# Performance work log

Measured on AMD Instinct MI355X. Metric: run time of the kernel, lower is better.

The kernel has to match this reference:

```python
import jax, jax.numpy as jnp
import numpy as np

NH, DH, DM = 16, 128, 2048
ROPE_THETA = 10000.0


def setup_inputs() -> dict:
    key = jax.random.key(0)
    k1, k2, k3 = jax.random.split(key, 3)
    x = jax.random.normal(k1, (2, 2048, DM), dtype=jnp.float32)
    w_qkv = jax.random.normal(k2, (3 * DM, DM), dtype=jnp.float32) * (DM ** -0.5)
    w_op = jax.random.normal(k3, (DM, DM), dtype=jnp.float32) * (DM ** -0.5)
    return {"x": x, "w_qkv": w_qkv, "w_op": w_op}


def _rope_tables(T, dtype):
    inv_freq = 1.0 / (ROPE_THETA ** (jnp.arange(0, DH, 2, dtype=jnp.float32) / DH))
    t = jnp.arange(T, dtype=jnp.float32)
    freqs = jnp.outer(t, inv_freq)              # (T, DH/2)
    emb = jnp.concatenate([freqs, freqs], axis=-1)  # (T, DH)
    cos = jnp.cos(emb)[None, :, None, :].astype(dtype)  # (1,T,1,DH)
    sin = jnp.sin(emb)[None, :, None, :].astype(dtype)
    return cos, sin


def _rotate_half(a):
    a1, a2 = a[..., : DH // 2], a[..., DH // 2 :]
    return jnp.concatenate([-a2, a1], axis=-1)


def reference(x, w_qkv, w_op):
    B, T, D = x.shape
    qkv = jnp.einsum('btd,ed->bte', x, w_qkv).reshape(B, T, 3, NH, DH)
    q, k, v = qkv[:, :, 0], qkv[:, :, 1], qkv[:, :, 2]  # (B,T,NH,DH)

    cos, sin = _rope_tables(T, x.dtype)
    q = q * cos + _rotate_half(q) * sin
    k = k * cos + _rotate_half(k) * sin

    # causal scaled dot-product attention
    scale = 1.0 / jnp.sqrt(jnp.asarray(DH, dtype=x.dtype))
    scores = jnp.einsum('bqhd,bkhd->bhqk', q, k) * scale  # (B,NH,T,T)
    causal = jnp.tril(jnp.ones((T, T), dtype=bool))
    scores = jnp.where(causal[None, None], scores, jnp.asarray(-1e30, dtype=x.dtype))
    attn = jax.nn.softmax(scores, axis=-1)
    out = jnp.einsum('bhqk,bkhd->bqhd', attn, v).reshape(B, T, D)
    return jnp.einsum('btd,ed->bte', out, w_op)
```

## Files before the change

### kernel.cpp

```cpp
#include <hip/hip_runtime.h>
#include <hip/hip_bf16.h>
#include <cstdint>

#define NHEAD 16
#define DHEAD 128
#define DMODEL 2048
#define TSEQ 2048
#define BATCH 2

using bf16 = __hip_bfloat16;
typedef __attribute__((ext_vector_type(4))) float  f32x4;
typedef __attribute__((ext_vector_type(2))) float  f32x2;
typedef __attribute__((ext_vector_type(4))) float  float4_t;
typedef __attribute__((ext_vector_type(4))) short  s16x4;
typedef __bf16 bf16x8 __attribute__((ext_vector_type(8)));

#define GLOAD_LDS16(gptr, lptr)                                                        \
  __builtin_amdgcn_global_load_lds((const __attribute__((address_space(1))) void*)(gptr), \
                                   (__attribute__((address_space(3))) void*)(lptr), 16, 0, 0)

#if __has_builtin(__builtin_amdgcn_exp2f)
#define EXP2(x) __builtin_amdgcn_exp2f(x)
#else
#define EXP2(x) exp2f(x)
#endif

__device__ __forceinline__ float bf2f(bf16 v) { return __bfloat162float(v); }
__device__ __forceinline__ bf16  f2bf(float f) { return __float2bfloat16(f); }
__device__ __forceinline__ unsigned short bfbits(float f) {
  return __builtin_bit_cast(unsigned short, f2bf(f));
}
__device__ __forceinline__ unsigned int pack2(float a, float b) {
  return (unsigned int)bfbits(a) | ((unsigned int)bfbits(b) << 16);
}

__global__ void cast_f32_to_bf16(const float* __restrict__ in, unsigned short* __restrict__ out, int n4) {
  int stride = gridDim.x * blockDim.x;
  for (int i = blockIdx.x * blockDim.x + threadIdx.x; i < n4; i += stride) {
    float4_t v = reinterpret_cast<const float4_t*>(in)[i];
    s16x4 r;
    r.x = (short)bfbits(v.x);
    r.y = (short)bfbits(v.y);
    r.z = (short)bfbits(v.z);
    r.w = (short)bfbits(v.w);
    reinterpret_cast<s16x4*>(out)[i] = r;
  }
}

__global__ void rope_tables(f32x2* __restrict__ cstab) {
  int i = blockIdx.x * blockDim.x + threadIdx.x;
  if (i >= TSEQ * 64) return;
  int t = i >> 6, f = i & 63;
  float inv = __expf(-((2.0f * (float)f) / 128.0f) * logf(10000.0f));
  float ang = (float)t * inv;
  f32x2 cs;
  cs.x = cosf(ang);
  cs.y = sinf(ang);
  cstab[i] = cs;
}

__global__ void transpose_v(const unsigned short* __restrict__ qkv, unsigned short* __restrict__ vt) {
  __shared__ short tile[64][132];
  const int bh = blockIdx.y;
  const int b = bh >> 4, h = bh & 15;
  const int t0 = blockIdx.x * 64;
  const int tid = threadIdx.x;
#pragma unroll
  for (int p = 0; p < 8; ++p) {
    int row  = p * 8 + (tid >> 5);
    int col  = (tid & 31) * 4;
    const unsigned short* src = qkv + (size_t)(b * TSEQ + t0 + row) * (3 * DMODEL) + 2 * DMODEL + h * DHEAD + col;
    s16x4 v = *reinterpret_cast<const s16x4*>(src);
    *reinterpret_cast<s16x4*>(&tile[row][col]) = v;
  }
  __syncthreads();
#pragma unroll
  for (int q = 0; q < 8; ++q) {
    int idx = q * 256 + tid;
    int d = idx >> 4, tq = idx & 15;
    s16x4 r;
    r.x = tile[tq * 4 + 0][d];
    r.y = tile[tq * 4 + 1][d];
    r.z = tile[tq * 4 + 2][d];
    r.w = tile[tq * 4 + 3][d];
    *reinterpret_cast<s16x4*>(vt + (size_t)(bh * DHEAD + d) * TSEQ + t0 + tq * 4) = r;
  }
}

__device__ __forceinline__ void store_c(float* p, float v) { *p = v; }
__device__ __forceinline__ void store_c(unsigned short* p, float v) { *p = bfbits(v); }

template <typename CT, bool ROPE>
__global__ __launch_bounds__(256, 2) void gemm_bt(const unsigned short* __restrict__ A,
                                                  const unsigned short* __restrict__ B,
                                                  CT* __restrict__ C, int M, int N, int K,
                                                  const f32x2* __restrict__ cstab) {
  __shared__ unsigned short As[128 * 32];
  __shared__ unsigned short Bs[128 * 32];
  const int tid  = threadIdx.x;
  const int wave = tid >> 6, lane = tid & 63;
  const int m0 = blockIdx.x * 128, n0 = blockIdx.y * 128;
  const int wm = wave * 32;
  const int lrow = lane >> 4, lcol = lane & 15;
  f32x4 acc[2][8] = {};

  for (int k0 = 0; k0 < K; k0 += 32) {
#pragma unroll
    for (int it = 0; it < 2; ++it) {
      int chunk = wave * 2 + it;
      int eoff  = chunk * 512 + lane * 8;
      int row   = eoff >> 5, col = eoff & 31;
      GLOAD_LDS16(A + (size_t)(m0 + row) * K + k0 + col, As + chunk * 512);
      GLOAD_LDS16(B + (size_t)(n0 + row) * K + k0 + col, Bs + chunk * 512);
    }
    __syncthreads();
    bf16x8 af[2], bfr[8];
#pragma unroll
    for (int mi = 0; mi < 2; ++mi)
      af[mi] = *reinterpret_cast<const bf16x8*>(&As[(wm + mi * 16 + lcol) * 32 + lrow * 8]);
#pragma unroll
    for (int ni = 0; ni < 8; ++ni)
      bfr[ni] = *reinterpret_cast<const bf16x8*>(&Bs[(ni * 16 + lcol) * 32 + lrow * 8]);
#pragma unroll
    for (int mi = 0; mi < 2; ++mi)
#pragma unroll
      for (int ni = 0; ni < 8; ++ni)
        acc[mi][ni] = __builtin_amdgcn_mfma_f32_16x16x32_bf16(af[mi], bfr[ni], acc[mi][ni], 0, 0, 0);
    __syncthreads();
  }

  if (ROPE && n0 < 2 * DMODEL) {
    const float qsc = (n0 < DMODEL) ? 0.12751743f : 1.0f;
#pragma unroll
    for (int mi = 0; mi < 2; ++mi)
#pragma unroll
      for (int j = 0; j < 4; ++j) {
        const int r = m0 + wm + mi * 16 + lrow * 4 + j;
        const int t = r & (TSEQ - 1);
#pragma unroll
        for (int ni = 0; ni < 4; ++ni) {
          const int f = ni * 16 + lcol;
          const f32x2 cs = cstab[t * 64 + f];
          const float a1 = acc[mi][ni][j];
          const float a2 = acc[mi][ni + 4][j];
          store_c(C + (size_t)r * N + n0 + f,      (a1 * cs.x - a2 * cs.y) * qsc);
          store_c(C + (size_t)r * N + n0 + f + 64, (a2 * cs.x + a1 * cs.y) * qsc);
        }
      }
  } else {
#pragma unroll
    for (int mi = 0; mi < 2; ++mi)
#pragma unroll
      for (int ni = 0; ni < 8; ++ni)
#pragma unroll
        for (int j = 0; j < 4; ++j) {
          int r = m0 + wm + mi * 16 + lrow * 4 + j;
          int c = n0 + ni * 16 + lcol;
          store_c(C + (size_t)r * N + c, acc[mi][ni][j]);
        }
  }
}

__global__ __launch_bounds__(512, 4) void flash_attn(const unsigned short* __restrict__ qkv,
                                                     const unsigned short* __restrict__ vt,
                                                     unsigned short* __restrict__ out) {
  __shared__ unsigned short kb[2][64 * 128];
  __shared__ unsigned short vb[2][128 * 64];
  __shared__ unsigned short plds[8][16 * 64];

  const int tid  = threadIdx.x;
  const int wave = tid >> 6, lane = tid & 63;
  const int lrow = lane >> 4, lcol = lane & 15;
  const int h = blockIdx.y, b = blockIdx.z;
  const int q0b = blockIdx.x * 128;
  const int q0w = q0b + wave * 16;
  const size_t qkbase = (size_t)b * TSEQ * (3 * DMODEL);
  const unsigned short* kptr = qkv + qkbase + DMODEL + h * DHEAD;
  const unsigned short* vptr = vt + (size_t)((b * NHEAD + h) * DHEAD) * TSEQ;

  bf16x8 qf[4];
#pragma unroll
  for (int kk = 0; kk < 4; ++kk)
    qf[kk] = *reinterpret_cast<const bf16x8*>(
        qkv + qkbase + (size_t)(q0w + lcol) * (3 * DMODEL) + h * DHEAD + kk * 32 + lrow * 8);

  f32x4 o[8] = {};
  float m = -1.0e30f, l = 0.f;

  const int nsteps = 2 * blockIdx.x + 2;

#define STAGE_KV(bi, kv0s)                                                              \
  {                                                                                     \
    _Pragma("unroll")                                                                   \
    for (int c = 0; c < 2; ++c) {                                                       \
      int cc = c * 512 + tid;                                                           \
      int krow = cc >> 4, kchk = (cc & 15) ^ (krow & 7);                                \
      GLOAD_LDS16(kptr + (size_t)((kv0s) + krow) * (3 * DMODEL) + kchk * 8,             \
                  &kb[bi][cc * 8]);                                                     \
      int vrow = cc >> 3, vchk = (cc & 7) ^ (vrow & 7);                                 \
      GLOAD_LDS16(vptr + (size_t)vrow * TSEQ + (kv0s) + vchk * 8,                       \
                  &vb[bi][cc * 8]);                                                     \
    }                                                                                   \
  }

  STAGE_KV(0, 0);
  __syncthreads();

  int cur = 0;
  for (int s = 0; s < nsteps; ++s) {
    const int kv0 = s * 64;
    if (s + 1 < nsteps) STAGE_KV(cur ^ 1, kv0 + 64);

    if (kv0 <= q0w + 15) {
      const unsigned short* kbc = kb[cur];
      const unsigned short* vbc = vb[cur];

      f32x4 sc[4] = {};
      __builtin_amdgcn_s_setprio(1);
#pragma unroll
      for (int n = 0; n < 4; ++n) {
        const int r = n * 16 + lcol;
#pragma unroll
        for (int kk = 0; kk < 4; ++kk) {
          bf16x8 kf = *reinterpret_cast<const bf16x8*>(
              &kbc[r * 128 + (((kk * 4 + lrow) ^ (lcol & 7)) << 3)]);
          sc[n] = __builtin_amdgcn_mfma_f32_16x16x32_bf16(kf, qf[kk], sc[n], 0, 0, 0);
        }
      }
      __builtin_amdgcn_s_setprio(0);

      const bool diag = (kv0 + 63 > q0w);
      const int qi = q0w + lcol;
      float sv[16];
#pragma unroll
      for (int n = 0; n < 4; ++n)
#pragma unroll
        for (int j = 0; j < 4; ++j) {
          float v = sc[n][j];
          if (diag && (kv0 + n * 16 + lrow * 4 + j) > qi) v = -1.0e30f;
          sv[n * 4 + j] = v;
        }
      float t8[8];
#pragma unroll
      for (int j = 0; j < 8; ++j) t8[j] = fmaxf(sv[j], sv[j + 8]);
#pragma unroll
      for (int j = 0; j < 4; ++j) t8[j] = fmaxf(t8[j], t8[j + 4]);
      float pm = fmaxf(fmaxf(t8[0], t8[1]), fmaxf(t8[2], t8[3]));
      pm = fmaxf(pm, __shfl_xor(pm, 16));
      pm = fmaxf(pm, __shfl_xor(pm, 32));

      if (__any(pm > m + 11.5f)) {
        const float mn  = fmaxf(m, pm);
        const float fsc = EXP2(m - mn);
        m = mn;
        l *= fsc;
#pragma unroll
        for (int c = 0; c < 8; ++c) o[c] *= fsc;
      }

#pragma unroll
      for (int i = 0; i < 16; ++i) sv[i] = EXP2(sv[i] - m);
      float a8[8];
#pragma unroll
      for (int j = 0; j < 8; ++j) a8[j] = sv[j] + sv[j + 8];
#pragma unroll
      for (int j = 0; j < 4; ++j) a8[j] += a8[j + 4];
      float rs = (a8[0] + a8[1]) + (a8[2] + a8[3]);
      rs += __shfl_xor(rs, 16);
      rs += __shfl_xor(rs, 32);
      l += rs;

      char* pw = reinterpret_cast<char*>(&plds[wave][0]);
#pragma unroll
      for (int n = 0; n < 4; ++n)
#pragma unroll
        for (int j = 0; j < 4; j += 2) {
          int boff = (lcol << 7) + ((((n << 1) + (lrow >> 1)) ^ (lcol & 7)) << 4) +
                     ((lrow & 1) << 3) + (j << 1);
          *reinterpret_cast<unsigned int*>(pw + boff) = pack2(sv[n * 4 + j], sv[n * 4 + j + 1]);
        }
      asm volatile("s_waitcnt lgkmcnt(0)" ::: "memory");

      bf16x8 pf0 = *reinterpret_cast<const bf16x8*>(
          pw + (lcol << 7) + ((lrow ^ (lcol & 7)) << 4));
      bf16x8 pf1 = *reinterpret_cast<const bf16x8*>(
          pw + (lcol << 7) + (((4 + lrow) ^ (lcol & 7)) << 4));

      __builtin_amdgcn_s_setprio(1);
#pragma unroll
      for (int c = 0; c < 8; ++c) {
        const int d = c * 16 + lcol;
        bf16x8 vf0 = *reinterpret_cast<const bf16x8*>(
            &vbc[d * 64 + ((lrow ^ (lcol & 7)) << 3)]);
        o[c] = __builtin_amdgcn_mfma_f32_16x16x32_bf16(vf0, pf0, o[c], 0, 0, 0);
        bf16x8 vf1 = *reinterpret_cast<const bf16x8*>(
            &vbc[d * 64 + (((4 + lrow) ^ (lcol & 7)) << 3)]);
        o[c] = __builtin_amdgcn_mfma_f32_16x16x32_bf16(vf1, pf1, o[c], 0, 0, 0);
      }
      __builtin_amdgcn_s_setprio(0);
    }

    __syncthreads();
    cur ^= 1;
  }

  const float rl = 1.0f / l;
  const int trow = q0w + lcol;
#pragma unroll
  for (int c = 0; c < 8; ++c) {
    s16x4 st;
#pragma unroll
    for (int j = 0; j < 4; ++j) st[j] = (short)bfbits(o[c][j] * rl);
    *reinterpret_cast<s16x4*>(
        out + (size_t)(b * TSEQ + trow) * DMODEL + h * DHEAD + c * 16 + lrow * 4) = st;
  }
#undef STAGE_KV
}

extern "C" void kernel_launch(void* const* d_in, const int* in_sizes, int n_in,
                              void* d_out, int out_size, void* d_ws, size_t ws_size,
                              hipStream_t stream) {
  const float* x     = (const float*)d_in[0];
  const float* w_qkv = (const float*)d_in[1];
  const float* w_op  = (const float*)d_in[2];
  float* out = (float*)d_out;

  const size_t SZ_XB  = (size_t)4096 * 2048 * 2;
  const size_t SZ_WQ  = (size_t)6144 * 2048 * 2;
  const size_t SZ_WO  = (size_t)2048 * 2048 * 2;
  const size_t SZ_QKV = (size_t)4096 * 6144 * 2;
  const size_t SZ_VT  = (size_t)32 * 128 * 2048 * 2;
  const size_t SZ_AO  = (size_t)4096 * 2048 * 2;
  const size_t SZ_TAB = (size_t)2048 * 64 * 8;
  const size_t NEEDED = SZ_XB + SZ_WQ + SZ_WO + SZ_QKV + SZ_VT + SZ_AO + SZ_TAB;
  if (ws_size < NEEDED) return;

  char* p = (char*)d_ws;
  unsigned short* xb   = (unsigned short*)p; p += SZ_XB;
  unsigned short* wqb  = (unsigned short*)p; p += SZ_WQ;
  unsigned short* wob  = (unsigned short*)p; p += SZ_WO;
  unsigned short* qkv  = (unsigned short*)p; p += SZ_QKV;
  unsigned short* vt   = (unsigned short*)p; p += SZ_VT;
  unsigned short* ao   = (unsigned short*)p; p += SZ_AO;
  f32x2* cstab = (f32x2*)p; p += SZ_TAB;

  cast_f32_to_bf16<<<dim3(2048), dim3(256), 0, stream>>>(x, xb, 4096 * 2048 / 4);
  cast_f32_to_bf16<<<dim3(2048), dim3(256), 0, stream>>>(w_qkv, wqb, 6144 * 2048 / 4);
  cast_f32_to_bf16<<<dim3(2048), dim3(256), 0, stream>>>(w_op, wob, 2048 * 2048 / 4);
  rope_tables<<<dim3(512), dim3(256), 0, stream>>>(cstab);

  gemm_bt<unsigned short, true><<<dim3(32, 48), dim3(256), 0, stream>>>(
      xb, wqb, qkv, 4096, 6144, 2048, cstab);
  transpose_v<<<dim3(32, 32), dim3(256), 0, stream>>>(qkv, vt);
  flash_attn<<<dim3(16, 16, 2), dim3(512), 0, stream>>>(qkv, vt, ao);
  gemm_bt<float, false><<<dim3(32, 16), dim3(256), 0, stream>>>(
      ao, wob, out, 4096, 2048, 2048, nullptr);
}
```

Baseline: 304.3 us.

## Replace QKV projection GEMM with 256x256 double-buffered ping-pong kernel

```diff
diff --git a/kernel.cpp b/kernel.cpp
--- a/kernel.cpp
+++ b/kernel.cpp
@@ -91,10 +91,177 @@
 __device__ __forceinline__ void store_c(unsigned short* p, float v) { *p = bfbits(v); }
 
 template <typename CT, bool ROPE>
-__global__ __launch_bounds__(256, 2) void gemm_bt(const unsigned short* __restrict__ A,
+__global__ __launch_bounds__(512, 2) void gemm_8p(const unsigned short* __restrict__ A,
                                                   const unsigned short* __restrict__ B,
                                                   CT* __restrict__ C, int M, int N, int K,
                                                   const f32x2* __restrict__ cstab) {
+  __shared__ __align__(16) unsigned short As[2][256 * 64];
+  __shared__ __align__(16) unsigned short Bs[2][256 * 64];
+
+  const int tid  = threadIdx.x;
+  const int lane = tid & 63;
+  const int wave = tid >> 6;
+  const int lrow = lane >> 4, lcol = lane & 15;
+  const int wm2 = wave >> 2, wn4 = wave & 3;
+
+  const int cpx = gridDim.x >> 3;
+  const int bid = (blockIdx.x & 7) * cpx + (blockIdx.x >> 3);
+  const int nby = N >> 8;
+  const int m0 = (bid / nby) * 256;
+  const int n0 = (bid % nby) * 256;
+  const int NT = K >> 6;
+
+  f32x4 acc[8][4] = {};
+
+#define STAGE_M(MAT, DST, slot, k0)                                          \
+  {                                                                          \
+    _Pragma("unroll")                                                        \
+    for (int it_ = 0; it_ < 4; ++it_) {                                      \
+      int CC_ = it_ * 512 + tid;                                             \
+      int R_ = CC_ >> 3, c_ = CC_ & 7;                                       \
+      GLOAD_LDS16(MAT + (size_t)((DST) + R_) * K + (k0) + ((c_ ^ (R_ & 7)) << 3), \
+                  (char*)(&slot[0]) + CC_ * 16);                             \
+    }                                                                        \
+  }
+
+#define RD_FRAG(BASE, R, ks)                                                 \
+  (*reinterpret_cast<const bf16x8*>(                                         \
+      (BASE) + (R) * 128 + (((((ks) << 2) + lrow) ^ (lcol & 7)) << 4)))
+
+  STAGE_M(A, m0, As[0], 0);
+  STAGE_M(B, n0, Bs[0], 0);
+  __syncthreads();
+
+  for (int t = 0; t < NT; ++t) {
+    const char* Ab = (const char*)(&As[t & 1][0]);
+    const char* Bb = (const char*)(&Bs[t & 1][0]);
+    const bool pf = (t + 1 < NT);
+    const int psl = (t + 1) & 1;
+    const int pk0 = (t + 1) << 6;
+
+    bf16x8 af[4][2], bfr[2][2];
+
+#pragma unroll
+    for (int mf = 0; mf < 4; ++mf)
+#pragma unroll
+      for (int ks = 0; ks < 2; ++ks)
+        af[mf][ks] = RD_FRAG(Ab, wm2 * 128 + mf * 16 + lcol, ks);
+#pragma unroll
+    for (int si = 0; si < 2; ++si)
+#pragma unroll
+      for (int ks = 0; ks < 2; ++ks)
+        bfr[si][ks] = RD_FRAG(Bb, (wn4 + 4 * si) * 16 + lcol, ks);
+    if (pf) STAGE_M(A, m0, As[psl], pk0);
+    __builtin_amdgcn_s_barrier();
+    __builtin_amdgcn_sched_barrier(0);
+    __builtin_amdgcn_s_setprio(1);
+#pragma unroll
+    for (int mf = 0; mf < 4; ++mf)
+#pragma unroll
+      for (int si = 0; si < 2; ++si)
+#pragma unroll
+        for (int ks = 0; ks < 2; ++ks)
+          acc[mf][si] = __builtin_amdgcn_mfma_f32_16x16x32_bf16(af[mf][ks], bfr[si][ks], acc[mf][si], 0, 0, 0);
+    __builtin_amdgcn_s_setprio(0);
+    __builtin_amdgcn_s_barrier();
+    __builtin_amdgcn_sched_barrier(0);
+
+#pragma unroll
+    for (int si = 0; si < 2; ++si)
+#pragma unroll
+      for (int ks = 0; ks < 2; ++ks)
+        bfr[si][ks] = RD_FRAG(Bb, (wn4 + 4 * (2 + si)) * 16 + lcol, ks);
+    if (pf) STAGE_M(B, n0, Bs[psl], pk0);
+    __builtin_amdgcn_s_barrier();
+    __builtin_amdgcn_sched_barrier(0);
+    __builtin_amdgcn_s_setprio(1);
+#pragma unroll
+    for (int mf = 0; mf < 4; ++mf)
+#pragma unroll
+      for (int si = 0; si < 2; ++si)
+#pragma unroll
+        for (int ks = 0; ks < 2; ++ks)
+          acc[mf][2 + si] = __builtin_amdgcn_mfma_f32_16x16x32_bf16(af[mf][ks], bfr[si][ks], acc[mf][2 + si], 0, 0, 0);
+    __builtin_amdgcn_s_setprio(0);
+    __builtin_amdgcn_s_barrier();
+    __builtin_amdgcn_sched_barrier(0);
+
+#pragma unroll
+    for (int mf = 0; mf < 4; ++mf)
+#pragma unroll
+      for (int ks = 0; ks < 2; ++ks)
+        af[mf][ks] = RD_FRAG(Ab, wm2 * 128 + (4 + mf) * 16 + lcol, ks);
+    __builtin_amdgcn_s_barrier();
+    __builtin_amdgcn_sched_barrier(0);
+    __builtin_amdgcn_s_setprio(1);
+#pragma unroll
+    for (int mf = 0; mf < 4; ++mf)
+#pragma unroll
+      for (int si = 0; si < 2; ++si)
+#pragma unroll
+        for (int ks = 0; ks < 2; ++ks)
+          acc[4 + mf][2 + si] = __builtin_amdgcn_mfma_f32_16x16x32_bf16(af[mf][ks], bfr[si][ks], acc[4 + mf][2 + si], 0, 0, 0);
+    __builtin_amdgcn_s_setprio(0);
+    __builtin_amdgcn_s_barrier();
+    __builtin_amdgcn_sched_barrier(0);
+
+#pragma unroll
+    for (int si = 0; si < 2; ++si)
+#pragma unroll
+      for (int ks = 0; ks < 2; ++ks)
+        bfr[si][ks] = RD_FRAG(Bb, (wn4 + 4 * si) * 16 + lcol, ks);
+    __builtin_amdgcn_s_barrier();
+    __builtin_amdgcn_sched_barrier(0);
+    __builtin_amdgcn_s_setprio(1);
+#pragma unroll
+    for (int mf = 0; mf < 4; ++mf)
+#pragma unroll
+      for (int si = 0; si < 2; ++si)
+#pragma unroll
+        for (int ks = 0; ks < 2; ++ks)
+          acc[4 + mf][si] = __builtin_amdgcn_mfma_f32_16x16x32_bf16(af[mf][ks], bfr[si][ks], acc[4 + mf][si], 0, 0, 0);
+    __builtin_amdgcn_s_setprio(0);
+
+    __syncthreads();
+  }
+#undef STAGE_M
+#undef RD_FRAG
+
+  if (ROPE && n0 < 2 * DMODEL) {
+    const float qsc = (n0 < DMODEL) ? 0.12751743f : 1.0f;
+    const int f = wn4 * 16 + lcol;
+#pragma unroll
+    for (int mi = 0; mi < 8; ++mi)
+#pragma unroll
+      for (int j = 0; j < 4; ++j) {
+        const int r = m0 + wm2 * 128 + mi * 16 + lrow * 4 + j;
+        const int t = r & (TSEQ - 1);
+        const f32x2 cs = cstab[t * 64 + f];
+        const float a1 = acc[mi][0][j], a2 = acc[mi][1][j];
+        store_c(C + (size_t)r * N + n0 + f,       (a1 * cs.x - a2 * cs.y) * qsc);
+        store_c(C + (size_t)r * N + n0 + f + 64,  (a2 * cs.x + a1 * cs.y) * qsc);
+        const float b1 = acc[mi][2][j], b2 = acc[mi][3][j];
+        store_c(C + (size_t)r * N + n0 + f + 128, (b1 * cs.x - b2 * cs.y) * qsc);
+        store_c(C + (size_t)r * N + n0 + f + 192, (b2 * cs.x + b1 * cs.y) * qsc);
+      }
+  } else {
+#pragma unroll
+    for (int mi = 0; mi < 8; ++mi)
+#pragma unroll
+      for (int si = 0; si < 4; ++si)
+#pragma unroll
+        for (int j = 0; j < 4; ++j) {
+          const int r = m0 + wm2 * 128 + mi * 16 + lrow * 4 + j;
+          const int c = n0 + (wn4 + 4 * si) * 16 + lcol;
+          store_c(C + (size_t)r * N + c, acc[mi][si][j]);
+        }
+  }
+}
+
+template <typename CT>
+__global__ __launch_bounds__(256, 2) void gemm_bt(const unsigned short* __restrict__ A,
+                                                  const unsigned short* __restrict__ B,
+                                                  CT* __restrict__ C, int M, int N, int K) {
   __shared__ unsigned short As[128 * 32];
   __shared__ unsigned short Bs[128 * 32];
   const int tid  = threadIdx.x;
@@ -128,37 +295,16 @@
         acc[mi][ni] = __builtin_amdgcn_mfma_f32_16x16x32_bf16(af[mi], bfr[ni], acc[mi][ni], 0, 0, 0);
     __syncthreads();
   }
-
-  if (ROPE && n0 < 2 * DMODEL) {
-    const float qsc = (n0 < DMODEL) ? 0.12751743f : 1.0f;
-#pragma unroll
-    for (int mi = 0; mi < 2; ++mi)
+#pragma unroll
+  for (int mi = 0; mi < 2; ++mi)
+#pragma unroll
+    for (int ni = 0; ni < 8; ++ni)
 #pragma unroll
       for (int j = 0; j < 4; ++j) {
-        const int r = m0 + wm + mi * 16 + lrow * 4 + j;
-        const int t = r & (TSEQ - 1);
-#pragma unroll
-        for (int ni = 0; ni < 4; ++ni) {
-          const int f = ni * 16 + lcol;
-          const f32x2 cs = cstab[t * 64 + f];
-          const float a1 = acc[mi][ni][j];
-          const float a2 = acc[mi][ni + 4][j];
-          store_c(C + (size_t)r * N + n0 + f,      (a1 * cs.x - a2 * cs.y) * qsc);
-          store_c(C + (size_t)r * N + n0 + f + 64, (a2 * cs.x + a1 * cs.y) * qsc);
-        }
+        int r = m0 + wm + mi * 16 + lrow * 4 + j;
+        int c = n0 + ni * 16 + lcol;
+        store_c(C + (size_t)r * N + c, acc[mi][ni][j]);
       }
-  } else {
-#pragma unroll
-    for (int mi = 0; mi < 2; ++mi)
-#pragma unroll
-      for (int ni = 0; ni < 8; ++ni)
-#pragma unroll
-        for (int j = 0; j < 4; ++j) {
-          int r = m0 + wm + mi * 16 + lrow * 4 + j;
-          int c = n0 + ni * 16 + lcol;
-          store_c(C + (size_t)r * N + c, acc[mi][ni][j]);
-        }
-  }
 }
 
 __global__ __launch_bounds__(512, 4) void flash_attn(const unsigned short* __restrict__ qkv,
@@ -349,10 +495,9 @@
   cast_f32_to_bf16<<<dim3(2048), dim3(256), 0, stream>>>(w_op, wob, 2048 * 2048 / 4);
   rope_tables<<<dim3(512), dim3(256), 0, stream>>>(cstab);
 
-  gemm_bt<unsigned short, true><<<dim3(32, 48), dim3(256), 0, stream>>>(
+  gemm_8p<unsigned short, true><<<dim3(384), dim3(512), 0, stream>>>(
       xb, wqb, qkv, 4096, 6144, 2048, cstab);
   transpose_v<<<dim3(32, 32), dim3(256), 0, stream>>>(qkv, vt);
   flash_attn<<<dim3(16, 16, 2), dim3(512), 0, stream>>>(qkv, vt, ao);
-  gemm_bt<float, false><<<dim3(32, 16), dim3(256), 0, stream>>>(
-      ao, wob, out, 4096, 2048, 2048, nullptr);
-}
+  gemm_bt<float><<<dim3(32, 16), dim3(256), 0, stream>>>(ao, wob, out, 4096, 2048, 2048);
+}
```

New measurement: 300.8 us. About the same (-1.1%).
